# Optimization experiments

Measured on AMD Instinct MI355X. Metric: run time of the kernel, lower is better.

Reference implementation:

```python
import jax, jax.numpy as jnp
import numpy as np

B, T, D = 4, 256, 1024
E, DL, TOPK, H = 16, 64, 2, 4


def setup_inputs() -> dict:
    key = jax.random.key(0)
    ks = jax.random.split(key, 12)
    n = lambda k, s: (0.02 * jax.random.normal(k, s)).astype(jnp.float32)
    return dict(
        x=jax.random.normal(ks[0], (B, T, D), dtype=jnp.float32),
        w_down=n(ks[1], (E * DL, D)),
        pos_embed=n(ks[2], (1, E, DL)),
        gp_w=n(ks[3], (DL, D)), gp_b=jnp.zeros((DL,), jnp.float32),
        attn_in_w=n(ks[4], (3 * DL, DL)), attn_in_b=jnp.zeros((3 * DL,), jnp.float32),
        attn_out_w=n(ks[5], (DL, DL)), attn_out_b=jnp.zeros((DL,), jnp.float32),
        ln_w=jnp.ones((DL,), jnp.float32), ln_b=jnp.zeros((DL,), jnp.float32),
        ls_w=n(ks[6], (1, DL)), ls_b=jnp.zeros((1,), jnp.float32),
        g1_w=n(ks[7], (2 * DL, DL)), g1_b=jnp.zeros((2 * DL,), jnp.float32),
        g2_w=n(ks[8], (E, 2 * DL)), g2_b=jnp.zeros((E,), jnp.float32),
        w_up=n(ks[9], (E, DL, D)),
    )


def reference(x, w_down, pos_embed, gp_w, gp_b, attn_in_w, attn_in_b,
              attn_out_w, attn_out_b, ln_w, ln_b, ls_w, ls_b,
              g1_w, g1_b, g2_w, g2_b, w_up):
    Bq, Tq, Dm = x.shape
    N = Bq * Tq
    xf = x.reshape(N, Dm)
    # per-token per-expert low-rank features [N, E, DL]
    ef = (xf @ w_down.T).reshape(N, E, DL)
    # global context per batch element -> [B, DL]
    gctx = x.mean(axis=1) @ gp_w.T + gp_b
    gtok = jnp.repeat(gctx, Tq, axis=0)[:, None, :]  # [N, 1, DL]
    seq = jnp.concatenate([gtok, ef + pos_embed], axis=1)  # [N, E+1, DL]
    # tiny multihead self-attention over E+1 tokens, eval mode (no dropout)
    qkv = seq @ attn_in_w.T + attn_in_b
    q, k, v = jnp.split(qkv, 3, axis=-1)
    hd = DL // H
    sh = lambda t: t.reshape(N, E + 1, H, hd).transpose(0, 2, 1, 3)
    q, k, v = sh(q), sh(k), sh(v)
    scores = jnp.einsum('nhqd,nhkd->nhqk', q, k) / np.float32(np.sqrt(hd))
    attn = jax.nn.softmax(scores, axis=-1)
    ctx = jnp.einsum('nhqk,nhkd->nhqd', attn, v).transpose(0, 2, 1, 3).reshape(N, E + 1, DL)
    attn_out = ctx @ attn_out_w.T + attn_out_b
    h = attn_out + seq
    mu = h.mean(-1, keepdims=True)
    var = h.var(-1, keepdims=True)
    hn = (h - mu) / jnp.sqrt(var + 1e-5) * ln_w + ln_b
    refined = hn[:, 1:, :]  # drop global token -> [N, E, DL]
    local_logits = (refined @ ls_w.T + ls_b)[..., 0]  # [N, E]
    gb = jax.nn.gelu(gctx @ g1_w.T + g1_b, approximate=False) @ g2_w.T + g2_b  # [B, E]
    logits = local_logits + jnp.repeat(gb, Tq, axis=0)
    probs = jax.nn.softmax(logits, axis=-1)
    tw, ti = jax.lax.top_k(probs, TOPK)
    tw = tw / tw.sum(-1, keepdims=True)
    sel = jnp.take_along_axis(ef, ti[..., None], axis=1)  # [N, K, DL]
    act = jax.nn.gelu(sel, approximate=False)
    # gather per-token expert up-projections and batched vec-mat
    eo = jnp.einsum('nkd,nkdm->nkm', act, w_up[ti])  # [N, K, D]
    out = (eo * tw[..., None]).sum(axis=1).reshape(Bq, Tq, Dm)
    mean_prob = probs.mean(axis=0)
    one_hot = jnp.zeros_like(probs).at[jnp.arange(N)[:, None], ti].set(1.0)
    aux_loss = E * jnp.sum(mean_prob * one_hot.mean(axis=0))
    return out, aux_loss
```

## Files before the change

### kernel.cpp

```cpp
#include <hip/hip_runtime.h>
#include <math.h>

#define NB 4
#define TT 256
#define DMODEL 1024
#define NE 16
#define DLQ 64
#define NH 4
#define HD 16
#define SEQL 17
#define NTOK 1024

static constexpr size_t WS_EF    = 0;
static constexpr size_t WS_AH    = 1048576;
static constexpr size_t WS_ACT   = 1048576;
static constexpr size_t WS_AL    = 1572864;
static constexpr size_t WS_BH    = 2097152;
static constexpr size_t WS_BL    = 2621440;
static constexpr size_t WS_WUPT  = 3145728;
static constexpr size_t WS_AIWFH = 3670016;
static constexpr size_t WS_AIWFL = 3676160;
static constexpr size_t WS_AOWFH = 3682304;
static constexpr size_t WS_AOWFL = 3684352;
static constexpr size_t WS_XPART = 4194304;
static constexpr size_t WS_PR    = 4194304;
static constexpr size_t WS_TI    = 4210688;
static constexpr size_t WS_GCTX  = 4227072;
static constexpr size_t WS_GB    = 4227328;

typedef __attribute__((ext_vector_type(8))) short short8;
typedef __attribute__((ext_vector_type(4))) float f32x4;

__device__ __forceinline__ float gelu_exact(float x) {
    return 0.5f * x * (1.0f + erff(x * 0.70710678118654752f));
}

__device__ __forceinline__ unsigned short f2bf(float f) {
    unsigned int u = __float_as_uint(f);
    unsigned int r = (u + 0x7fffu + ((u >> 16) & 1u)) >> 16;
    return (unsigned short)r;
}
__device__ __forceinline__ float bf2f(unsigned short h) {
    return __uint_as_float(((unsigned int)h) << 16);
}

#define DPP_ADD(v, ctrl) { int _m = __builtin_amdgcn_update_dpp(0, __float_as_int(v), ctrl, 0xF, 0xF, true); \
                           v += __int_as_float(_m); }
__device__ __forceinline__ float rsum16(float v) {
    DPP_ADD(v, 0x128);
    DPP_ADD(v, 0x124);
    DPP_ADD(v, 0x122);
    DPP_ADD(v, 0x121);
    return v;
}
__device__ __forceinline__ float rsum64(float v) {
    v = rsum16(v);
    v += __shfl_xor(v, 16);
    v += __shfl_xor(v, 32);
    return v;
}

__global__ __launch_bounds__(256) void k_prep(const float* __restrict__ x,
                                              const float* __restrict__ wdn,
                                              const float* __restrict__ w_up,
                                              const float* __restrict__ aiw,
                                              const float* __restrict__ aow,
                                              float* __restrict__ ws) {
    __shared__ float tile[64][65];
    int bi = blockIdx.x;
    int tid = threadIdx.x;
    if (bi < 1024) {
        int which = bi >> 9;
        int t = (bi & 511) * 256 + tid;
        int row = t >> 7;
        int col0 = (t & 127) * 8;
        const float* src = which ? wdn : x;
        unsigned short* hp = (unsigned short*)(ws + (which ? WS_BH : WS_AH));
        unsigned short* lp = (unsigned short*)(ws + (which ? WS_BL : WS_AL));
        float4 v0 = *(const float4*)(src + (size_t)row * DMODEL + col0);
        float4 v1 = *(const float4*)(src + (size_t)row * DMODEL + col0 + 4);
        float vv[8] = {v0.x, v0.y, v0.z, v0.w, v1.x, v1.y, v1.z, v1.w};
        unsigned short h8[8], l8[8];
#pragma unroll
        for (int j = 0; j < 8; ++j) {
            h8[j] = f2bf(vv[j]);
            l8[j] = f2bf(vv[j] - bf2f(h8[j]));
        }
        int nb = row >> 6, kb = col0 >> 6;
        int st = (row & 63) >> 4;
        int ks = (col0 & 63) >> 5;
        int ln = (row & 15) + (((col0 >> 3) & 3) << 4);
        size_t off = (size_t)(nb * 16 + kb) * 4096 + st * 1024 + ks * 512 + ln * 8;
        *(short8*)(hp + off) = *(short8*)h8;
        *(short8*)(lp + off) = *(short8*)l8;
    } else if (bi < 1280) {
        int e = (bi - 1024) >> 4, ct = (bi - 1024) & 15;
#pragma unroll
        for (int jj = 0; jj < 16; ++jj) {
            int j = jj * 4 + (tid >> 6);
            tile[j][tid & 63] = w_up[((size_t)e * DLQ + j) * DMODEL + ct * 64 + (tid & 63)];
        }
        __syncthreads();
        int c = tid >> 2, j0 = (tid & 3) * 16;
        unsigned short* dst = (unsigned short*)(ws + WS_WUPT) +
                              (size_t)e * 65536 + (size_t)(ct * 64 + c) * 64 + j0;
#pragma unroll
        for (int q = 0; q < 4; ++q) {
            ushort4 o;
            o.x = f2bf(tile[j0 + q * 4 + 0][c]);
            o.y = f2bf(tile[j0 + q * 4 + 1][c]);
            o.z = f2bf(tile[j0 + q * 4 + 2][c]);
            o.w = f2bf(tile[j0 + q * 4 + 3][c]);
            *(ushort4*)(dst + q * 4) = o;
        }
    } else {
        unsigned short* fh = (unsigned short*)(ws + WS_AIWFH);
        unsigned short* fl = (unsigned short*)(ws + WS_AIWFL);
        for (int idx = tid; idx < 12 * 2 * 64; idx += 256) {
            int nt = idx >> 7, kf = (idx >> 6) & 1, l = idx & 63;
            int row = nt * 16 + (l & 15);
            int k = kf * 32 + ((l >> 4) << 3);
            const float* src = aiw + (size_t)row * DLQ + k;
            unsigned short h8[8], l8[8];
#pragma unroll
            for (int j = 0; j < 8; ++j) {
                h8[j] = f2bf(src[j]);
                l8[j] = f2bf(src[j] - bf2f(h8[j]));
            }
            size_t off = (size_t)(nt * 2 + kf) * 512 + l * 8;
            *(short8*)(fh + off) = *(short8*)h8;
            *(short8*)(fl + off) = *(short8*)l8;
        }
        unsigned short* gh = (unsigned short*)(ws + WS_AOWFH);
        unsigned short* gl = (unsigned short*)(ws + WS_AOWFL);
        for (int idx = tid; idx < 4 * 2 * 64; idx += 256) {
            int nt = idx >> 7, kf = (idx >> 6) & 1, l = idx & 63;
            int row = nt * 16 + (l & 15);
            int k = kf * 32 + ((l >> 4) << 3);
            const float* src = aow + (size_t)row * DLQ + k;
            unsigned short h8[8], l8[8];
#pragma unroll
            for (int j = 0; j < 8; ++j) {
                h8[j] = f2bf(src[j]);
                l8[j] = f2bf(src[j] - bf2f(h8[j]));
            }
            size_t off = (size_t)(nt * 2 + kf) * 512 + l * 8;
            *(short8*)(gh + off) = *(short8*)h8;
            *(short8*)(gl + off) = *(short8*)l8;
        }
    }
}

__global__ __launch_bounds__(256) void k_batch_partial(const float* __restrict__ x,
                                                       float* __restrict__ ws) {
    int b = blockIdx.x >> 3;
    int g = blockIdx.x & 7;
    int tid = threadIdx.x;
    const float* xp = x + (size_t)b * TT * DMODEL + (size_t)g * 32 * DMODEL + tid * 4;
    float4 acc = {0.f, 0.f, 0.f, 0.f};
#pragma unroll 4
    for (int t = 0; t < 32; ++t) {
        float4 v = *(const float4*)(xp + (size_t)t * DMODEL);
        acc.x += v.x; acc.y += v.y; acc.z += v.z; acc.w += v.w;
    }
    *(float4*)(ws + WS_XPART + (size_t)blockIdx.x * DMODEL + tid * 4) = acc;
}

__global__ __launch_bounds__(256) void k_global_ctx(const float* __restrict__ gp_w,
                                                    const float* __restrict__ gp_b,
                                                    const float* __restrict__ g1_w,
                                                    const float* __restrict__ g1_b,
                                                    const float* __restrict__ g2_w,
                                                    const float* __restrict__ g2_b,
                                                    float* __restrict__ ws) {
    int b = blockIdx.x, tid = threadIdx.x;
    __shared__ float xm[DMODEL];
    __shared__ float gc[DLQ];
    __shared__ float gb1[128];
    float4 a = {0.f, 0.f, 0.f, 0.f};
#pragma unroll
    for (int g = 0; g < 8; ++g) {
        float4 v = *(const float4*)(ws + WS_XPART + (size_t)(b * 8 + g) * DMODEL + tid * 4);
        a.x += v.x; a.y += v.y; a.z += v.z; a.w += v.w;
    }
    const float inv_t = 1.0f / (float)TT;
    xm[tid * 4 + 0] = a.x * inv_t;
    xm[tid * 4 + 1] = a.y * inv_t;
    xm[tid * 4 + 2] = a.z * inv_t;
    xm[tid * 4 + 3] = a.w * inv_t;
    __syncthreads();
    if (tid < DLQ) {
        const float* wr = gp_w + (size_t)tid * DMODEL;
        float s = 0.f;
        for (int j = 0; j < DMODEL; j += 4) {
            float4 w4 = *(const float4*)(wr + j);
            float4 x4 = *(const float4*)&xm[j];
            s += w4.x * x4.x + w4.y * x4.y + w4.z * x4.z + w4.w * x4.w;
        }
        float v = s + gp_b[tid];
        gc[tid] = v;
        ws[WS_GCTX + b * DLQ + tid] = v;
    }
    __syncthreads();
    if (tid < 128) {
        const float* wr = g1_w + (size_t)tid * DLQ;
        float s = 0.f;
        for (int j = 0; j < DLQ; j += 4) {
            float4 w4 = *(const float4*)(wr + j);
            float4 x4 = *(const float4*)&gc[j];
            s += w4.x * x4.x + w4.y * x4.y + w4.z * x4.z + w4.w * x4.w;
        }
        gb1[tid] = gelu_exact(s + g1_b[tid]);
    }
    __syncthreads();
    if (tid < NE) {
        const float* wr = g2_w + (size_t)tid * 128;
        float s = 0.f;
        for (int j = 0; j < 128; ++j) s += wr[j] * gb1[j];
        ws[WS_GB + b * NE + tid] = s + g2_b[tid];
    }
}

__global__ __launch_bounds__(256) void k_ef_mfma(float* __restrict__ ws) {
    __shared__ __attribute__((aligned(16))) unsigned short smem[16384];
    const unsigned short* AhP = (const unsigned short*)(ws + WS_AH);
    const unsigned short* AlP = (const unsigned short*)(ws + WS_AL);
    const unsigned short* BhP = (const unsigned short*)(ws + WS_BH);
    const unsigned short* BlP = (const unsigned short*)(ws + WS_BL);
    int tid = threadIdx.x;
    int mb = blockIdx.x;
    int nb = blockIdx.y;
    int w = tid >> 6, l = tid & 63;
    int wn = (w >> 1) * 32, wm = (w & 1) * 32;
    int stA = wn >> 4, stB = wm >> 4;
    f32x4 acc00 = {0.f, 0.f, 0.f, 0.f}, acc01 = acc00, acc10 = acc00, acc11 = acc00;

    for (int kb = 0; kb < 16; ++kb) {
        const char* srcs[4] = {
            (const char*)(AhP + (size_t)(nb * 16 + kb) * 4096),
            (const char*)(AlP + (size_t)(nb * 16 + kb) * 4096),
            (const char*)(BhP + (size_t)(mb * 16 + kb) * 4096),
            (const char*)(BlP + (size_t)(mb * 16 + kb) * 4096)};
#pragma unroll
        for (int p = 0; p < 4; ++p) {
#pragma unroll
            for (int h = 0; h < 2; ++h) {
                __builtin_amdgcn_global_load_lds(
                    (const __attribute__((address_space(1))) void*)(srcs[p] + h * 4096 + tid * 16),
                    (__attribute__((address_space(3))) void*)((char*)smem + p * 8192 + h * 4096 + tid * 16),
                    16, 0, 0);
            }
        }
        __syncthreads();
        const unsigned short* Ah = smem;
        const unsigned short* Al = smem + 4096;
        const unsigned short* Bh = smem + 8192;
        const unsigned short* Bl = smem + 12288;
#pragma unroll
        for (int ks = 0; ks < 2; ++ks) {
            short8 ah0 = *(const short8*)(Ah + (stA + 0) * 1024 + ks * 512 + l * 8);
            short8 ah1 = *(const short8*)(Ah + (stA + 1) * 1024 + ks * 512 + l * 8);
            short8 al0 = *(const short8*)(Al + (stA + 0) * 1024 + ks * 512 + l * 8);
            short8 al1 = *(const short8*)(Al + (stA + 1) * 1024 + ks * 512 + l * 8);
            short8 bh0 = *(const short8*)(Bh + (stB + 0) * 1024 + ks * 512 + l * 8);
            short8 bh1 = *(const short8*)(Bh + (stB + 1) * 1024 + ks * 512 + l * 8);
            short8 bl0 = *(const short8*)(Bl + (stB + 0) * 1024 + ks * 512 + l * 8);
            short8 bl1 = *(const short8*)(Bl + (stB + 1) * 1024 + ks * 512 + l * 8);
            acc00 = __builtin_amdgcn_mfma_f32_16x16x32_bf16(ah0, bh0, acc00, 0, 0, 0);
            acc00 = __builtin_amdgcn_mfma_f32_16x16x32_bf16(al0, bh0, acc00, 0, 0, 0);
            acc00 = __builtin_amdgcn_mfma_f32_16x16x32_bf16(ah0, bl0, acc00, 0, 0, 0);
            acc01 = __builtin_amdgcn_mfma_f32_16x16x32_bf16(ah0, bh1, acc01, 0, 0, 0);
            acc01 = __builtin_amdgcn_mfma_f32_16x16x32_bf16(al0, bh1, acc01, 0, 0, 0);
            acc01 = __builtin_amdgcn_mfma_f32_16x16x32_bf16(ah0, bl1, acc01, 0, 0, 0);
            acc10 = __builtin_amdgcn_mfma_f32_16x16x32_bf16(ah1, bh0, acc10, 0, 0, 0);
            acc10 = __builtin_amdgcn_mfma_f32_16x16x32_bf16(al1, bh0, acc10, 0, 0, 0);
            acc10 = __builtin_amdgcn_mfma_f32_16x16x32_bf16(ah1, bl0, acc10, 0, 0, 0);
            acc11 = __builtin_amdgcn_mfma_f32_16x16x32_bf16(ah1, bh1, acc11, 0, 0, 0);
            acc11 = __builtin_amdgcn_mfma_f32_16x16x32_bf16(al1, bh1, acc11, 0, 0, 0);
            acc11 = __builtin_amdgcn_mfma_f32_16x16x32_bf16(ah1, bl1, acc11, 0, 0, 0);
        }
        __syncthreads();
    }
    int cr = (l >> 4) * 4, cc = l & 15;
    int n0 = nb * 64, m0 = mb * 64;
    float* P = ws + WS_EF;
#pragma unroll
    for (int r = 0; r < 4; ++r) {
        P[(size_t)(n0 + wn + cr + r) * DMODEL + (m0 + wm + cc)]           = acc00[r];
        P[(size_t)(n0 + wn + cr + r) * DMODEL + (m0 + wm + 16 + cc)]      = acc01[r];
        P[(size_t)(n0 + wn + 16 + cr + r) * DMODEL + (m0 + wm + cc)]      = acc10[r];
        P[(size_t)(n0 + wn + 16 + cr + r) * DMODEL + (m0 + wm + 16 + cc)] = acc11[r];
    }
}

__global__ __launch_bounds__(128) void k_attn2(const float* __restrict__ pos_embed,
                                               const float* __restrict__ attn_in_b,
                                               const float* __restrict__ attn_out_b,
                                               const float* __restrict__ ln_w,
                                               const float* __restrict__ ln_b,
                                               const float* __restrict__ ls_w,
                                               const float* __restrict__ ls_b,
                                               float* __restrict__ ws) {
    int n = blockIdx.x;
    int w = threadIdx.x >> 6;
    int l = threadIdx.x & 63;
    int b = n >> 8;

    __shared__ float qkv[SEQL * 200];
    __shared__ __attribute__((aligned(16))) char ubuf[8192];
    __shared__ __attribute__((aligned(16))) unsigned short ctxH[1024];
    __shared__ __attribute__((aligned(16))) unsigned short ctxL[1024];
    __shared__ float lgv_sh[NE];
    unsigned short* sH = (unsigned short*)ubuf;
    unsigned short* sL = (unsigned short*)(ubuf + 4096);
    float* ao = (float*)ubuf;

    float seqc[SEQL];
    {
        const float* efp = ws + WS_EF + (size_t)n * DMODEL;
        float gcv = ws[WS_GCTX + b * DLQ + l];
#pragma unroll
        for (int i = 0; i < SEQL; ++i) {
            float s = (i == 0) ? gcv : efp[(i - 1) * DLQ + l] + pos_embed[(i - 1) * DLQ + l];
            seqc[i] = s;
            int lo_r = w * 9, hi_r = w * 9 + 8;
            if (i >= lo_r && i <= hi_r && i < SEQL) {
                unsigned short hs = f2bf(s);
                unsigned short lsv = f2bf(s - bf2f(hs));
                int mt = i >> 4;
                int ls = (i & 15) + (((l >> 3) & 3) << 4);
                int kf = l >> 5;
                int j = l & 7;
                size_t off = (size_t)(mt * 2 + kf) * 512 + ls * 8 + j;
                sH[off] = hs;
                sL[off] = lsv;
            }
        }
    }
    __syncthreads();

    {
        const unsigned short* fh = (const unsigned short*)(ws + WS_AIWFH);
        const unsigned short* fl = (const unsigned short*)(ws + WS_AIWFL);
        f32x4 acc[6][2];
#pragma unroll
        for (int t = 0; t < 6; ++t)
#pragma unroll
            for (int m = 0; m < 2; ++m) acc[t][m] = (f32x4){0.f, 0.f, 0.f, 0.f};
#pragma unroll
        for (int kf = 0; kf < 2; ++kf) {
            short8 ah0 = *(const short8*)(sH + (0 * 2 + kf) * 512 + l * 8);
            short8 ah1 = *(const short8*)(sH + (1 * 2 + kf) * 512 + l * 8);
            short8 al0 = *(const short8*)(sL + (0 * 2 + kf) * 512 + l * 8);
            short8 al1 = *(const short8*)(sL + (1 * 2 + kf) * 512 + l * 8);
#pragma unroll
            for (int t = 0; t < 6; ++t) {
                int nt = w * 6 + t;
                short8 bh = *(const short8*)(fh + (size_t)(nt * 2 + kf) * 512 + l * 8);
                short8 bl = *(const short8*)(fl + (size_t)(nt * 2 + kf) * 512 + l * 8);
                acc[t][0] = __builtin_amdgcn_mfma_f32_16x16x32_bf16(ah0, bh, acc[t][0], 0, 0, 0);
                acc[t][0] = __builtin_amdgcn_mfma_f32_16x16x32_bf16(al0, bh, acc[t][0], 0, 0, 0);
                acc[t][0] = __builtin_amdgcn_mfma_f32_16x16x32_bf16(ah0, bl, acc[t][0], 0, 0, 0);
                acc[t][1] = __builtin_amdgcn_mfma_f32_16x16x32_bf16(ah1, bh, acc[t][1], 0, 0, 0);
                acc[t][1] = __builtin_amdgcn_mfma_f32_16x16x32_bf16(al1, bh, acc[t][1], 0, 0, 0);
                acc[t][1] = __builtin_amdgcn_mfma_f32_16x16x32_bf16(ah1, bl, acc[t][1], 0, 0, 0);
            }
        }
#pragma unroll
        for (int t = 0; t < 6; ++t) {
            int col = (w * 6 + t) * 16 + (l & 15);
            float bias = attn_in_b[col];
#pragma unroll
            for (int r = 0; r < 4; ++r) {
                int row = (l >> 4) * 4 + r;
                qkv[row * 200 + col] = acc[t][0][r] + bias;
            }
            if ((l >> 4) == 0) qkv[16 * 200 + col] = acc[t][1][0] + bias;
        }
    }
    __syncthreads();

    {
        int g = l >> 4;
        float kc[SEQL], vc[SEQL];
#pragma unroll
        for (int j = 0; j < SEQL; ++j) {
            kc[j] = qkv[j * 200 + 64 + g * 16 + (l & 15)];
            vc[j] = qkv[j * 200 + 128 + l];
        }
        for (int i = w * 8 + 1; i <= w * 8 + 8; ++i) {
            float qi = qkv[i * 200 + g * 16 + (l & 15)];
            float sj[SEQL];
#pragma unroll
            for (int j = 0; j < SEQL; ++j) {
                sj[j] = rsum16(qi * kc[j]) * 0.25f;
            }
            float m = sj[0];
#pragma unroll
            for (int j = 1; j < SEQL; ++j) m = fmaxf(m, sj[j]);
            float ssum = 0.f;
#pragma unroll
            for (int j = 0; j < SEQL; ++j) { sj[j] = __expf(sj[j] - m); ssum += sj[j]; }
            float inv = 1.f / ssum;
            float c = 0.f;
#pragma unroll
            for (int j = 0; j < SEQL; ++j) c += sj[j] * vc[j];
            c *= inv;
            unsigned short ch = f2bf(c);
            unsigned short cl = f2bf(c - bf2f(ch));
            int ls = ((i - 1) & 15) + (((l >> 3) & 3) << 4);
            int kf = l >> 5;
            int j2 = l & 7;
            size_t off = (size_t)kf * 512 + ls * 8 + j2;
            ctxH[off] = ch;
            ctxL[off] = cl;
        }
    }
    __syncthreads();

    {
        const unsigned short* gh = (const unsigned short*)(ws + WS_AOWFH);
        const unsigned short* gl = (const unsigned short*)(ws + WS_AOWFL);
        f32x4 acc[2];
        acc[0] = (f32x4){0.f, 0.f, 0.f, 0.f};
        acc[1] = acc[0];
#pragma unroll
        for (int kf = 0; kf < 2; ++kf) {
            short8 ah = *(const short8*)(ctxH + kf * 512 + l * 8);
            short8 al = *(const short8*)(ctxL + kf * 512 + l * 8);
#pragma unroll
            for (int t = 0; t < 2; ++t) {
                int nt = w * 2 + t;
                short8 bh = *(const short8*)(gh + (size_t)(nt * 2 + kf) * 512 + l * 8);
                short8 bl = *(const short8*)(gl + (size_t)(nt * 2 + kf) * 512 + l * 8);
                acc[t] = __builtin_amdgcn_mfma_f32_16x16x32_bf16(ah, bh, acc[t], 0, 0, 0);
                acc[t] = __builtin_amdgcn_mfma_f32_16x16x32_bf16(al, bh, acc[t], 0, 0, 0);
                acc[t] = __builtin_amdgcn_mfma_f32_16x16x32_bf16(ah, bl, acc[t], 0, 0, 0);
            }
        }
        __syncthreads();
#pragma unroll
        for (int t = 0; t < 2; ++t) {
            int col = (w * 2 + t) * 16 + (l & 15);
            float bias = attn_out_b[col];
#pragma unroll
            for (int r = 0; r < 4; ++r) {
                int row = (l >> 4) * 4 + r;
                ao[row * 72 + col] = acc[t][r] + bias;
            }
        }
    }
    __syncthreads();

    float rs[SEQL];
#pragma unroll
    for (int i = 1; i < SEQL; ++i) rs[i] = seqc[i] + ao[(i - 1) * 72 + l];

    float c1 = ln_w[l] * ls_w[l];
    float c1sum = rsum64(c1);
    float c0sum = rsum64(ln_b[l] * ls_w[l]);
    float lsb0 = ls_b[0];
#pragma unroll
    for (int ee = 0; ee < 8; ++ee) {
        int e = w * 8 + ee;
        float x = rs[e + 1];
        float s1 = rsum64(x);
        float s2 = rsum64(x * x);
        float s3 = rsum64(x * c1);
        float mu = s1 * (1.0f / DLQ);
        float var = s2 * (1.0f / DLQ) - mu * mu;
        float rstd = rsqrtf(var + 1e-5f);
        float lgv = rstd * (s3 - mu * c1sum) + c0sum + lsb0 + ws[WS_GB + b * NE + e];
        if (l == 0) lgv_sh[e] = lgv;
    }
    __syncthreads();

    if (w == 0) {
        float p[NE];
        float lgv[NE];
#pragma unroll
        for (int e = 0; e < NE; ++e) lgv[e] = lgv_sh[e];
        float m = lgv[0];
#pragma unroll
        for (int e = 1; e < NE; ++e) m = fmaxf(m, lgv[e]);
        float ssum = 0.f;
#pragma unroll
        for (int e = 0; e < NE; ++e) { p[e] = __expf(lgv[e] - m); ssum += p[e]; }
        float inv = 1.f / ssum;
#pragma unroll
        for (int e = 0; e < NE; ++e) p[e] *= inv;
        int t0 = 0; float b0 = p[0];
#pragma unroll
        for (int e = 1; e < NE; ++e) if (p[e] > b0) { b0 = p[e]; t0 = e; }
        int t1 = -1; float b1 = -1.f;
#pragma unroll
        for (int e = 0; e < NE; ++e) if (e != t0 && p[e] > b1) { b1 = p[e]; t1 = e; }

        float sw = b0 + b1;
        float tw0 = b0 / sw, tw1 = b1 / sw;
        unsigned short* actp = (unsigned short*)(ws + WS_ACT);
        float efv0 = ws[WS_EF + (size_t)n * DMODEL + t0 * DLQ + l];
        float efv1 = ws[WS_EF + (size_t)n * DMODEL + t1 * DLQ + l];
        actp[(size_t)(n * 2 + 0) * 64 + l] = f2bf(gelu_exact(efv0) * tw0);
        actp[(size_t)(n * 2 + 1) * 64 + l] = f2bf(gelu_exact(efv1) * tw1);
        if (l == 0) {
#pragma unroll
            for (int e = 0; e < NE; ++e) ws[WS_PR + (size_t)n * NE + e] = p[e];
            ((int*)(ws + WS_TI))[n] = t0 | (t1 << 8);
        }
    }
}

__global__ __launch_bounds__(256) void k_moe_gemm(float* __restrict__ ws,
                                                  float* __restrict__ out) {
    __shared__ int lst[2048];
    __shared__ int lcnt;
    __shared__ float wsum[4][NE];
    __shared__ int hist[NE];
    int tid = threadIdx.x;
    int wv = tid >> 6, l = tid & 63;

    if (blockIdx.x == NE) {
        if (blockIdx.y != 0) return;
        if (tid < NE) hist[tid] = 0;
        __syncthreads();
        {
            const int* tip = (const int*)(ws + WS_TI);
#pragma unroll
            for (int c = 0; c < 4; ++c) {
                int pk = tip[tid * 4 + c];
                atomicAdd(&hist[pk & 0xff], 1);
                atomicAdd(&hist[(pk >> 8) & 0xff], 1);
            }
        }
        float p[NE];
#pragma unroll
        for (int e = 0; e < NE; ++e) p[e] = 0.f;
        const float* pr = ws + WS_PR + (size_t)tid * 64;
#pragma unroll
        for (int r = 0; r < 4; ++r)
#pragma unroll
            for (int q = 0; q < 4; ++q) {
                float4 v = *(const float4*)(pr + r * 16 + q * 4);
                p[q * 4 + 0] += v.x; p[q * 4 + 1] += v.y;
                p[q * 4 + 2] += v.z; p[q * 4 + 3] += v.w;
            }
#pragma unroll
        for (int e = 0; e < NE; ++e) p[e] = rsum64(p[e]);
        if (l == 0) {
#pragma unroll
            for (int e = 0; e < NE; ++e) wsum[wv][e] = p[e];
        }
        __syncthreads();
        if (tid == 0) {
            float s = 0.f;
#pragma unroll
            for (int e = 0; e < NE; ++e) {
                float sp = wsum[0][e] + wsum[1][e] + wsum[2][e] + wsum[3][e];
                s += sp * (float)hist[e];
            }
            out[(size_t)NTOK * DMODEL] = (float)NE * s / ((float)NTOK * (float)NTOK);
        }
        return;
    }

    int e = blockIdx.x, ct = blockIdx.y;
    if (tid == 0) lcnt = 0;
    __syncthreads();
    {
        const int* tip = (const int*)(ws + WS_TI);
#pragma unroll
        for (int c = 0; c < 4; ++c) {
            int tok = wv * 256 + c * 64 + l;
            int pk = tip[tok];
            bool m1 = ((pk >> 8) & 0xff) == e;
            bool m = ((pk & 0xff) == e) || m1;
            unsigned long long mask = __ballot(m);
            int base = 0;
            if (l == 0 && mask) base = atomicAdd(&lcnt, __popcll(mask));
            base = __shfl(base, 0);
            if (m) {
                int pos = base + __popcll(mask & ((1ull << l) - 1ull));
                lst[pos] = tok * 2 + (m1 ? 1 : 0);
            }
        }
    }
    __syncthreads();
    int cnt = lcnt;
    if (cnt == 0) return;

    const unsigned short* wupt = (const unsigned short*)(ws + WS_WUPT) + (size_t)e * 65536;
    const unsigned short* actp = (const unsigned short*)(ws + WS_ACT);
    int col = ct * 64 + wv * 16 + (l & 15);
    int kb = (l >> 4) * 8;
    short8 bf0 = *(const short8*)(wupt + (size_t)col * 64 + kb);
    short8 bf1 = *(const short8*)(wupt + (size_t)col * 64 + 32 + kb);
    int cr = (l >> 4) * 4;

    for (int mt = 0; mt < cnt; mt += 16) {
        int row = mt + (l & 15);
        short8 a0 = {0, 0, 0, 0, 0, 0, 0, 0};
        short8 a1 = {0, 0, 0, 0, 0, 0, 0, 0};
        if (row < cnt) {
            int pk = lst[row];
            a0 = *(const short8*)(actp + (size_t)pk * 64 + kb);
            a1 = *(const short8*)(actp + (size_t)pk * 64 + 32 + kb);
        }
        f32x4 acc = {0.f, 0.f, 0.f, 0.f};
        acc = __builtin_amdgcn_mfma_f32_16x16x32_bf16(a0, bf0, acc, 0, 0, 0);
        acc = __builtin_amdgcn_mfma_f32_16x16x32_bf16(a1, bf1, acc, 0, 0, 0);
#pragma unroll
        for (int r = 0; r < 4; ++r) {
            int rr = mt + cr + r;
            if (rr < cnt) {
                int pk = lst[rr];
                atomicAdd(&out[(size_t)(pk >> 1) * DMODEL + col], acc[r]);
            }
        }
    }
}

extern "C" void kernel_launch(void* const* d_in, const int* in_sizes, int n_in,
                              void* d_out, int out_size, void* d_ws, size_t ws_size,
                              hipStream_t stream) {
    const float* x          = (const float*)d_in[0];
    const float* w_down     = (const float*)d_in[1];
    const float* pos_embed  = (const float*)d_in[2];
    const float* gp_w       = (const float*)d_in[3];
    const float* gp_b       = (const float*)d_in[4];
    const float* attn_in_w  = (const float*)d_in[5];
    const float* attn_in_b  = (const float*)d_in[6];
    const float* attn_out_w = (const float*)d_in[7];
    const float* attn_out_b = (const float*)d_in[8];
    const float* ln_w       = (const float*)d_in[9];
    const float* ln_b       = (const float*)d_in[10];
    const float* ls_w       = (const float*)d_in[11];
    const float* ls_b       = (const float*)d_in[12];
    const float* g1_w       = (const float*)d_in[13];
    const float* g1_b       = (const float*)d_in[14];
    const float* g2_w       = (const float*)d_in[15];
    const float* g2_b       = (const float*)d_in[16];
    const float* w_up       = (const float*)d_in[17];
    float* ws  = (float*)d_ws;
    float* out = (float*)d_out;

    hipMemsetAsync(out, 0, (size_t)out_size * sizeof(float), stream);
    k_prep<<<1281, 256, 0, stream>>>(x, w_down, w_up, attn_in_w, attn_out_w, ws);
    k_batch_partial<<<32, 256, 0, stream>>>(x, ws);
    k_global_ctx<<<NB, 256, 0, stream>>>(gp_w, gp_b, g1_w, g1_b, g2_w, g2_b, ws);
    k_ef_mfma<<<dim3(16, 16), 256, 0, stream>>>(ws);
    k_attn2<<<NTOK, 128, 0, stream>>>(pos_embed, attn_in_b, attn_out_b,
                                      ln_w, ln_b, ls_w, ls_b, ws);
    k_moe_gemm<<<dim3(NE + 1, 16), 256, 0, stream>>>(ws, out);
}
```

Baseline: 186.5 us.

## Fuse small kernels, split-K the ef GEMM, and convert w_up inline in MoE GEMM

The batch-sum partial pass moves into the prep kernel and the global-context computation becomes an extra block of the ef MFMA kernel, cutting two launches. The ef GEMM is split along K into two halves written to separate buffers, which the attention kernel sums when it reads them, doubling the block count. The w_up transpose and bf16 conversion step is removed, and the MoE GEMM instead loads fp32 w_up with strided reads and converts it in registers. The trade-offs are uncoalesced strided loads of w_up, extra partial-buffer reads in the attention kernel, and a global-context block that runs serially over batches inside the GEMM grid.

```diff
diff --git a/kernel.cpp b/kernel.cpp
--- a/kernel.cpp
+++ b/kernel.cpp
@@ -13,20 +13,20 @@
 
 static constexpr size_t WS_EF    = 0;
 static constexpr size_t WS_AH    = 1048576;
-static constexpr size_t WS_ACT   = 1048576;
 static constexpr size_t WS_AL    = 1572864;
 static constexpr size_t WS_BH    = 2097152;
 static constexpr size_t WS_BL    = 2621440;
-static constexpr size_t WS_WUPT  = 3145728;
-static constexpr size_t WS_AIWFH = 3670016;
-static constexpr size_t WS_AIWFL = 3676160;
-static constexpr size_t WS_AOWFH = 3682304;
-static constexpr size_t WS_AOWFL = 3684352;
-static constexpr size_t WS_XPART = 4194304;
-static constexpr size_t WS_PR    = 4194304;
-static constexpr size_t WS_TI    = 4210688;
-static constexpr size_t WS_GCTX  = 4227072;
-static constexpr size_t WS_GB    = 4227328;
+static constexpr size_t WS_P1    = 3145728;
+static constexpr size_t WS_ACT   = 4194304;
+static constexpr size_t WS_AIWFH = 4259840;
+static constexpr size_t WS_AIWFL = 4265984;
+static constexpr size_t WS_AOWFH = 4272128;
+static constexpr size_t WS_AOWFL = 4274176;
+static constexpr size_t WS_XPART = 4276224;
+static constexpr size_t WS_PR    = 4308992;
+static constexpr size_t WS_TI    = 4325376;
+static constexpr size_t WS_GCTX  = 4326400;
+static constexpr size_t WS_GB    = 4326656;
 
 typedef __attribute__((ext_vector_type(8))) short short8;
 typedef __attribute__((ext_vector_type(4))) float f32x4;
@@ -62,11 +62,9 @@
 
 __global__ __launch_bounds__(256) void k_prep(const float* __restrict__ x,
                                               const float* __restrict__ wdn,
-                                              const float* __restrict__ w_up,
                                               const float* __restrict__ aiw,
                                               const float* __restrict__ aow,
                                               float* __restrict__ ws) {
-    __shared__ float tile[64][65];
     int bi = blockIdx.x;
     int tid = threadIdx.x;
     if (bi < 1024) {
@@ -93,26 +91,18 @@
         size_t off = (size_t)(nb * 16 + kb) * 4096 + st * 1024 + ks * 512 + ln * 8;
         *(short8*)(hp + off) = *(short8*)h8;
         *(short8*)(lp + off) = *(short8*)l8;
-    } else if (bi < 1280) {
-        int e = (bi - 1024) >> 4, ct = (bi - 1024) & 15;
-#pragma unroll
-        for (int jj = 0; jj < 16; ++jj) {
-            int j = jj * 4 + (tid >> 6);
-            tile[j][tid & 63] = w_up[((size_t)e * DLQ + j) * DMODEL + ct * 64 + (tid & 63)];
-        }
-        __syncthreads();
-        int c = tid >> 2, j0 = (tid & 3) * 16;
-        unsigned short* dst = (unsigned short*)(ws + WS_WUPT) +
-                              (size_t)e * 65536 + (size_t)(ct * 64 + c) * 64 + j0;
-#pragma unroll
-        for (int q = 0; q < 4; ++q) {
-            ushort4 o;
-            o.x = f2bf(tile[j0 + q * 4 + 0][c]);
-            o.y = f2bf(tile[j0 + q * 4 + 1][c]);
-            o.z = f2bf(tile[j0 + q * 4 + 2][c]);
-            o.w = f2bf(tile[j0 + q * 4 + 3][c]);
-            *(ushort4*)(dst + q * 4) = o;
-        }
+    } else if (bi < 1056) {
+        int sb = bi - 1024;
+        int b = sb >> 3;
+        int g = sb & 7;
+        const float* xp = x + (size_t)b * TT * DMODEL + (size_t)g * 32 * DMODEL + tid * 4;
+        float4 acc = {0.f, 0.f, 0.f, 0.f};
+#pragma unroll 4
+        for (int t = 0; t < 32; ++t) {
+            float4 v = *(const float4*)(xp + (size_t)t * DMODEL);
+            acc.x += v.x; acc.y += v.y; acc.z += v.z; acc.w += v.w;
+        }
+        *(float4*)(ws + WS_XPART + (size_t)sb * DMODEL + tid * 4) = acc;
     } else {
         unsigned short* fh = (unsigned short*)(ws + WS_AIWFH);
         unsigned short* fl = (unsigned short*)(ws + WS_AIWFL);
@@ -151,91 +141,83 @@
     }
 }
 
-__global__ __launch_bounds__(256) void k_batch_partial(const float* __restrict__ x,
-                                                       float* __restrict__ ws) {
-    int b = blockIdx.x >> 3;
-    int g = blockIdx.x & 7;
+__global__ __launch_bounds__(256) void k_ef_mfma(const float* __restrict__ gp_w,
+                                                 const float* __restrict__ gp_b,
+                                                 const float* __restrict__ g1_w,
+                                                 const float* __restrict__ g1_b,
+                                                 const float* __restrict__ g2_w,
+                                                 const float* __restrict__ g2_b,
+                                                 float* __restrict__ ws) {
+    __shared__ __attribute__((aligned(16))) unsigned short smem[16384];
     int tid = threadIdx.x;
-    const float* xp = x + (size_t)b * TT * DMODEL + (size_t)g * 32 * DMODEL + tid * 4;
-    float4 acc = {0.f, 0.f, 0.f, 0.f};
-#pragma unroll 4
-    for (int t = 0; t < 32; ++t) {
-        float4 v = *(const float4*)(xp + (size_t)t * DMODEL);
-        acc.x += v.x; acc.y += v.y; acc.z += v.z; acc.w += v.w;
-    }
-    *(float4*)(ws + WS_XPART + (size_t)blockIdx.x * DMODEL + tid * 4) = acc;
-}
-
-__global__ __launch_bounds__(256) void k_global_ctx(const float* __restrict__ gp_w,
-                                                    const float* __restrict__ gp_b,
-                                                    const float* __restrict__ g1_w,
-                                                    const float* __restrict__ g1_b,
-                                                    const float* __restrict__ g2_w,
-                                                    const float* __restrict__ g2_b,
-                                                    float* __restrict__ ws) {
-    int b = blockIdx.x, tid = threadIdx.x;
-    __shared__ float xm[DMODEL];
-    __shared__ float gc[DLQ];
-    __shared__ float gb1[128];
-    float4 a = {0.f, 0.f, 0.f, 0.f};
-#pragma unroll
-    for (int g = 0; g < 8; ++g) {
-        float4 v = *(const float4*)(ws + WS_XPART + (size_t)(b * 8 + g) * DMODEL + tid * 4);
-        a.x += v.x; a.y += v.y; a.z += v.z; a.w += v.w;
-    }
-    const float inv_t = 1.0f / (float)TT;
-    xm[tid * 4 + 0] = a.x * inv_t;
-    xm[tid * 4 + 1] = a.y * inv_t;
-    xm[tid * 4 + 2] = a.z * inv_t;
-    xm[tid * 4 + 3] = a.w * inv_t;
-    __syncthreads();
-    if (tid < DLQ) {
-        const float* wr = gp_w + (size_t)tid * DMODEL;
-        float s = 0.f;
-        for (int j = 0; j < DMODEL; j += 4) {
-            float4 w4 = *(const float4*)(wr + j);
-            float4 x4 = *(const float4*)&xm[j];
-            s += w4.x * x4.x + w4.y * x4.y + w4.z * x4.z + w4.w * x4.w;
-        }
-        float v = s + gp_b[tid];
-        gc[tid] = v;
-        ws[WS_GCTX + b * DLQ + tid] = v;
-    }
-    __syncthreads();
-    if (tid < 128) {
-        const float* wr = g1_w + (size_t)tid * DLQ;
-        float s = 0.f;
-        for (int j = 0; j < DLQ; j += 4) {
-            float4 w4 = *(const float4*)(wr + j);
-            float4 x4 = *(const float4*)&gc[j];
-            s += w4.x * x4.x + w4.y * x4.y + w4.z * x4.z + w4.w * x4.w;
-        }
-        gb1[tid] = gelu_exact(s + g1_b[tid]);
-    }
-    __syncthreads();
-    if (tid < NE) {
-        const float* wr = g2_w + (size_t)tid * 128;
-        float s = 0.f;
-        for (int j = 0; j < 128; ++j) s += wr[j] * gb1[j];
-        ws[WS_GB + b * NE + tid] = s + g2_b[tid];
-    }
-}
-
-__global__ __launch_bounds__(256) void k_ef_mfma(float* __restrict__ ws) {
-    __shared__ __attribute__((aligned(16))) unsigned short smem[16384];
+    int mb = blockIdx.x;
+    int nb = blockIdx.y;
+    int kz = blockIdx.z;
+
+    if (mb == 16) {
+        if (nb != 0 || kz != 0) return;
+        float* xm  = (float*)smem;
+        float* gc  = (float*)smem + 1024;
+        float* gb1 = (float*)smem + 1088;
+        for (int b = 0; b < NB; ++b) {
+            float4 a = {0.f, 0.f, 0.f, 0.f};
+#pragma unroll
+            for (int g = 0; g < 8; ++g) {
+                float4 v = *(const float4*)(ws + WS_XPART + (size_t)(b * 8 + g) * DMODEL + tid * 4);
+                a.x += v.x; a.y += v.y; a.z += v.z; a.w += v.w;
+            }
+            const float inv_t = 1.0f / (float)TT;
+            xm[tid * 4 + 0] = a.x * inv_t;
+            xm[tid * 4 + 1] = a.y * inv_t;
+            xm[tid * 4 + 2] = a.z * inv_t;
+            xm[tid * 4 + 3] = a.w * inv_t;
+            __syncthreads();
+            if (tid < DLQ) {
+                const float* wr = gp_w + (size_t)tid * DMODEL;
+                float s = 0.f;
+                for (int j = 0; j < DMODEL; j += 4) {
+                    float4 w4 = *(const float4*)(wr + j);
+                    float4 x4 = *(const float4*)&xm[j];
+                    s += w4.x * x4.x + w4.y * x4.y + w4.z * x4.z + w4.w * x4.w;
+                }
+                float v = s + gp_b[tid];
+                gc[tid] = v;
+                ws[WS_GCTX + b * DLQ + tid] = v;
+            }
+            __syncthreads();
+            if (tid < 128) {
+                const float* wr = g1_w + (size_t)tid * DLQ;
+                float s = 0.f;
+                for (int j = 0; j < DLQ; j += 4) {
+                    float4 w4 = *(const float4*)(wr + j);
+                    float4 x4 = *(const float4*)&gc[j];
+                    s += w4.x * x4.x + w4.y * x4.y + w4.z * x4.z + w4.w * x4.w;
+                }
+                gb1[tid] = gelu_exact(s + g1_b[tid]);
+            }
+            __syncthreads();
+            if (tid < NE) {
+                const float* wr = g2_w + (size_t)tid * 128;
+                float s = 0.f;
+                for (int j = 0; j < 128; ++j) s += wr[j] * gb1[j];
+                ws[WS_GB + b * NE + tid] = s + g2_b[tid];
+            }
+            __syncthreads();
+        }
+        return;
+    }
+
     const unsigned short* AhP = (const unsigned short*)(ws + WS_AH);
     const unsigned short* AlP = (const unsigned short*)(ws + WS_AL);
     const unsigned short* BhP = (const unsigned short*)(ws + WS_BH);
     const unsigned short* BlP = (const unsigned short*)(ws + WS_BL);
-    int tid = threadIdx.x;
-    int mb = blockIdx.x;
-    int nb = blockIdx.y;
     int w = tid >> 6, l = tid & 63;
     int wn = (w >> 1) * 32, wm = (w & 1) * 32;
     int stA = wn >> 4, stB = wm >> 4;
     f32x4 acc00 = {0.f, 0.f, 0.f, 0.f}, acc01 = acc00, acc10 = acc00, acc11 = acc00;
 
-    for (int kb = 0; kb < 16; ++kb) {
+    for (int it = 0; it < 8; ++it) {
+        int kb = kz * 8 + it;
         const char* srcs[4] = {
             (const char*)(AhP + (size_t)(nb * 16 + kb) * 4096),
             (const char*)(AlP + (size_t)(nb * 16 + kb) * 4096),
@@ -283,7 +265,7 @@
     }
     int cr = (l >> 4) * 4, cc = l & 15;
     int n0 = nb * 64, m0 = mb * 64;
-    float* P = ws + WS_EF;
+    float* P = ws + (kz == 0 ? WS_EF : WS_P1);
 #pragma unroll
     for (int r = 0; r < 4; ++r) {
         P[(size_t)(n0 + wn + cr + r) * DMODEL + (m0 + wm + cc)]           = acc00[r];
@@ -317,11 +299,14 @@
 
     float seqc[SEQL];
     {
-        const float* efp = ws + WS_EF + (size_t)n * DMODEL;
+        const float* efp0 = ws + WS_EF + (size_t)n * DMODEL;
+        const float* efp1 = ws + WS_P1 + (size_t)n * DMODEL;
         float gcv = ws[WS_GCTX + b * DLQ + l];
 #pragma unroll
         for (int i = 0; i < SEQL; ++i) {
-            float s = (i == 0) ? gcv : efp[(i - 1) * DLQ + l] + pos_embed[(i - 1) * DLQ + l];
+            float s = (i == 0) ? gcv
+                               : efp0[(i - 1) * DLQ + l] + efp1[(i - 1) * DLQ + l] +
+                                 pos_embed[(i - 1) * DLQ + l];
             seqc[i] = s;
             int lo_r = w * 9, hi_r = w * 9 + 8;
             if (i >= lo_r && i <= hi_r && i < SEQL) {
@@ -499,8 +484,10 @@
         float sw = b0 + b1;
         float tw0 = b0 / sw, tw1 = b1 / sw;
         unsigned short* actp = (unsigned short*)(ws + WS_ACT);
-        float efv0 = ws[WS_EF + (size_t)n * DMODEL + t0 * DLQ + l];
-        float efv1 = ws[WS_EF + (size_t)n * DMODEL + t1 * DLQ + l];
+        float efv0 = ws[WS_EF + (size_t)n * DMODEL + t0 * DLQ + l] +
+                     ws[WS_P1 + (size_t)n * DMODEL + t0 * DLQ + l];
+        float efv1 = ws[WS_EF + (size_t)n * DMODEL + t1 * DLQ + l] +
+                     ws[WS_P1 + (size_t)n * DMODEL + t1 * DLQ + l];
         actp[(size_t)(n * 2 + 0) * 64 + l] = f2bf(gelu_exact(efv0) * tw0);
         actp[(size_t)(n * 2 + 1) * 64 + l] = f2bf(gelu_exact(efv1) * tw1);
         if (l == 0) {
@@ -511,7 +498,8 @@
     }
 }
 
-__global__ __launch_bounds__(256) void k_moe_gemm(float* __restrict__ ws,
+__global__ __launch_bounds__(256) void k_moe_gemm(const float* __restrict__ w_up,
+                                                  float* __restrict__ ws,
                                                   float* __restrict__ out) {
     __shared__ int lst[2048];
     __shared__ int lcnt;
@@ -589,12 +577,19 @@
     int cnt = lcnt;
     if (cnt == 0) return;
 
-    const unsigned short* wupt = (const unsigned short*)(ws + WS_WUPT) + (size_t)e * 65536;
-    const unsigned short* actp = (const unsigned short*)(ws + WS_ACT);
     int col = ct * 64 + wv * 16 + (l & 15);
     int kb = (l >> 4) * 8;
-    short8 bf0 = *(const short8*)(wupt + (size_t)col * 64 + kb);
-    short8 bf1 = *(const short8*)(wupt + (size_t)col * 64 + 32 + kb);
+    const float* wue = w_up + (size_t)e * DLQ * DMODEL + col;
+    unsigned short b0v[8], b1v[8];
+#pragma unroll
+    for (int j = 0; j < 8; ++j) {
+        b0v[j] = f2bf(wue[(size_t)(kb + j) * DMODEL]);
+        b1v[j] = f2bf(wue[(size_t)(kb + 32 + j) * DMODEL]);
+    }
+    short8 bf0 = *(short8*)b0v;
+    short8 bf1 = *(short8*)b1v;
+
+    const unsigned short* actp = (const unsigned short*)(ws + WS_ACT);
     int cr = (l >> 4) * 4;
 
     for (int mt = 0; mt < cnt; mt += 16) {
@@ -645,11 +640,9 @@
     float* out = (float*)d_out;
 
     hipMemsetAsync(out, 0, (size_t)out_size * sizeof(float), stream);
-    k_prep<<<1281, 256, 0, stream>>>(x, w_down, w_up, attn_in_w, attn_out_w, ws);
-    k_batch_partial<<<32, 256, 0, stream>>>(x, ws);
-    k_global_ctx<<<NB, 256, 0, stream>>>(gp_w, gp_b, g1_w, g1_b, g2_w, g2_b, ws);
-    k_ef_mfma<<<dim3(16, 16), 256, 0, stream>>>(ws);
+    k_prep<<<1057, 256, 0, stream>>>(x, w_down, attn_in_w, attn_out_w, ws);
+    k_ef_mfma<<<dim3(17, 16, 2), 256, 0, stream>>>(gp_w, gp_b, g1_w, g1_b, g2_w, g2_b, ws);
     k_attn2<<<NTOK, 128, 0, stream>>>(pos_embed, attn_in_b, attn_out_b,
                                       ln_w, ln_b, ls_w, ls_b, ws);
-    k_moe_gemm<<<dim3(NE + 1, 16), 256, 0, stream>>>(ws, out);
-}
+    k_moe_gemm<<<dim3(NE + 1, 16), 256, 0, stream>>>(w_up, ws, out);
+}
```

Result: slower. 210.4 us (+12.8%).
